# Optimization experiments

Measured on AMD Instinct MI355X. Metric: run time of the kernel, lower is better.

Reference implementation:

```python
import jax, jax.numpy as jnp
import numpy as np

FACTOR = 5

def setup_inputs() -> dict:
    key = jax.random.key(0)
    k1, k2, k3, k4 = jax.random.split(key, 4)
    B, L, E = 64, 4096, 64
    sample_k = min(FACTOR * int(np.ceil(np.log(L))), L)  # 45
    return {
        "queries": jax.random.normal(k1, (B, L, E), dtype=jnp.float32),
        "keys": jax.random.normal(k2, (B, L, E), dtype=jnp.float32),
        "values": jax.random.normal(k3, (B, L, E), dtype=jnp.float32),
        "index_sample": jax.random.randint(k4, (L, sample_k), 0, L, dtype=jnp.int32),
    }

def reference(queries, keys, values, index_sample):
    B, L_Q, D = queries.shape
    _, L_K, _ = keys.shape
    u = min(FACTOR * int(np.ceil(np.log(L_Q))), L_Q)  # n_top queries

    # --- _prob_QK: random K-sample gather + sparsity measure + topk ---
    # K_sample: (B, L_Q, sample_k, E) via gather (no dense K_expand materialized)
    K_sample = keys[:, index_sample, :]
    Q_K_sample = jnp.einsum('ble,blse->bls', queries, K_sample)
    M = Q_K_sample.max(-1) - Q_K_sample.sum(-1) / L_K  # (B, L_Q)
    _, M_top = jax.lax.top_k(M, u)  # (B, u) indices of top queries

    Q_reduce = jnp.take_along_axis(queries, M_top[:, :, None], axis=1)  # (B, u, E)
    scores_top = jnp.einsum('bue,bke->buk', Q_reduce, keys)  # (B, u, L_K)

    scale = 1.0 / np.sqrt(D)
    scores_top = scores_top * scale

    # --- _get_initial_context: mask_flag=True -> cumulative sum of V ---
    context = jnp.cumsum(values, axis=-2)  # (B, L_Q, D)

    # --- _update_context: softmax over full keys, scatter into context rows ---
    attn = jax.nn.softmax(scores_top, axis=-1)  # (B, u, L_K)
    upd = jnp.einsum('buk,bkd->bud', attn, values)  # (B, u, D)
    context = context.at[jnp.arange(B)[:, None], M_top, :].set(upd)
    return context
```

## Files before the change

### kernel.cpp

```cpp
#include <hip/hip_runtime.h>

#define Bv 64
#define Lv 4096
#define Dv 64
#define Uv 45
#define UP 48
#define NC 16
#define CKK 256
#define NSUB 64

#define OFF_M    0
#define SZ_M     (Bv*Lv)
#define OFF_QR   (OFF_M + SZ_M)
#define SZ_QR    (Bv*UP*Dv)
#define OFF_PMS  (OFF_QR + SZ_QR)
#define SZ_PMS   (Bv*NC*2*UP)
#define OFF_DEN  (OFF_PMS + SZ_PMS)
#define SZ_DEN   (Bv*2*UP)
#define OFF_PPV  (OFF_DEN + SZ_DEN)
#define SZ_PPV   (Bv*NC*UP*Dv)
#define OFF_CS   (OFF_PPV + SZ_PPV)
#define SZ_CS    (Bv*NSUB*Dv)
#define OFF_CO   (OFF_CS + SZ_CS)
#define SZ_CO    (Bv*NSUB*Dv)
#define OFF_TOP  (OFF_CO + SZ_CO)
#define SZ_TOP   (Bv*Uv)

__global__ __launch_bounds__(256) void k_M(const float* __restrict__ Q,
                                           const float* __restrict__ K,
                                           const int* __restrict__ idx,
                                           float* __restrict__ Mout) {
  __shared__ int sidx[16 * Uv];
  int i = blockIdx.x;
  int x = i & 7, j = i >> 3;
  int b = x + 8 * (j >> 8);
  int w = j & 255;
  int t = threadIdx.x;
  for (int p = t; p < 16 * Uv; p += 256) sidx[p] = idx[w * (16 * Uv) + p];
  int g = t >> 4, lane = t & 15;
  int l = w * 16 + g;
  float4 qv = *(const float4*)(Q + ((size_t)b * Lv + l) * Dv + lane * 4);
  const float* Kb = K + (size_t)b * Lv * Dv + lane * 4;
  __syncthreads();
  float mx = -3.0e38f, sm = 0.f;
#pragma unroll 5
  for (int s = 0; s < Uv; s++) {
    int ki = sidx[g * Uv + s];
    float4 kv = *(const float4*)(Kb + (size_t)ki * Dv);
    float d = qv.x * kv.x + qv.y * kv.y + qv.z * kv.z + qv.w * kv.w;
    d += __shfl_xor(d, 1);
    d += __shfl_xor(d, 2);
    d += __shfl_xor(d, 4);
    d += __shfl_xor(d, 8);
    mx = fmaxf(mx, d);
    sm += d;
  }
  if (lane == 0) Mout[(size_t)b * Lv + l] = mx - sm * (1.0f / (float)Lv);
}

__global__ __launch_bounds__(256) void k_topk(const float* __restrict__ M,
                                              int* __restrict__ Mtop) {
  __shared__ float sv[Lv];
  __shared__ float rmax[256];
  __shared__ int rind[256];
  int b = blockIdx.x;
  const float* Mb = M + (size_t)b * Lv;
  for (int i = threadIdx.x; i < Lv; i += 256) sv[i] = Mb[i];
  __syncthreads();
  for (int it = 0; it < Uv; it++) {
    float best = -3.0e38f; int bi = 1 << 30;
    for (int i = threadIdx.x; i < Lv; i += 256) {
      float v = sv[i];
      if (v > best) { best = v; bi = i; }
    }
    rmax[threadIdx.x] = best; rind[threadIdx.x] = bi;
    __syncthreads();
    for (int off = 128; off > 0; off >>= 1) {
      if (threadIdx.x < off) {
        float v2 = rmax[threadIdx.x + off]; int i2 = rind[threadIdx.x + off];
        if (v2 > rmax[threadIdx.x] ||
            (v2 == rmax[threadIdx.x] && i2 < rind[threadIdx.x])) {
          rmax[threadIdx.x] = v2; rind[threadIdx.x] = i2;
        }
      }
      __syncthreads();
    }
    if (threadIdx.x == 0) { Mtop[b * Uv + it] = rind[0]; sv[rind[0]] = -3.0e38f; }
    __syncthreads();
  }
}

__global__ __launch_bounds__(256) void k_qstage(const float* __restrict__ Q,
                                                const int* __restrict__ Mtop,
                                                float* __restrict__ Qr) {
  int b = blockIdx.x;
  for (int i = threadIdx.x; i < UP * Dv; i += 256) {
    int u = i >> 6, e = i & 63;
    float v = 0.f;
    if (u < Uv) {
      int row = Mtop[b * Uv + u];
      v = Q[((size_t)b * Lv + row) * Dv + e] * 0.125f;
    }
    Qr[((size_t)b * UP + u) * Dv + e] = v;
  }
}

#define STAGE_QST(QS, QR, b)                                        \
  for (int i_ = threadIdx.x; i_ < Dv * UP; i_ += blockDim.x) {      \
    int u_ = i_ >> 6, e_ = i_ & 63;                                 \
    QS[e_ * UP + u_] = QR[((size_t)(b) * UP + u_) * Dv + e_];       \
  }

#define SCORE_TILE(ACC, QS, KMAT, b_, c_, ug_, kg_)                                   \
  {                                                                                    \
    const float* Kb_ = (KMAT) + ((size_t)(b_) * Lv + (size_t)(c_) * CKK + (kg_)) * Dv; \
    for (int e = 0; e < Dv; e += 4) {                                                  \
      float qq[4][8];                                                                  \
      _Pragma("unroll")                                                                \
      for (int e2 = 0; e2 < 4; e2++) {                                                 \
        float4 qa = *(const float4*)&(QS)[(e + e2) * UP + (ug_) * 8];                  \
        float4 qb = *(const float4*)&(QS)[(e + e2) * UP + (ug_) * 8 + 4];              \
        qq[e2][0]=qa.x; qq[e2][1]=qa.y; qq[e2][2]=qa.z; qq[e2][3]=qa.w;                \
        qq[e2][4]=qb.x; qq[e2][5]=qb.y; qq[e2][6]=qb.z; qq[e2][7]=qb.w;                \
      }                                                                                \
      _Pragma("unroll")                                                                \
      for (int j = 0; j < 8; j++) {                                                    \
        float4 kv = *(const float4*)(Kb_ + (size_t)(32 * j) * Dv + e);                 \
        _Pragma("unroll")                                                              \
        for (int uu = 0; uu < 8; uu++)                                                 \
          ACC[uu][j] += qq[0][uu]*kv.x + qq[1][uu]*kv.y + qq[2][uu]*kv.z + qq[3][uu]*kv.w; \
      }                                                                                  \
    }                                                                                  \
  }

__global__ __launch_bounds__(192) void k_ms(const float* __restrict__ Kmat,
                                            const float* __restrict__ Qr,
                                            float* __restrict__ pms) {
  __shared__ float qsT[Dv * UP];
  int b = blockIdx.x >> 4, c = blockIdx.x & 15;
  STAGE_QST(qsT, Qr, b);
  __syncthreads();
  int t = threadIdx.x, ug = t >> 5, kg = t & 31;
  float acc[8][8];
#pragma unroll
  for (int uu = 0; uu < 8; uu++)
#pragma unroll
    for (int j = 0; j < 8; j++) acc[uu][j] = 0.f;
  SCORE_TILE(acc, qsT, Kmat, b, c, ug, kg);
#pragma unroll
  for (int uu = 0; uu < 8; uu++) {
    float m = acc[uu][0];
#pragma unroll
    for (int j = 1; j < 8; j++) m = fmaxf(m, acc[uu][j]);
#pragma unroll
    for (int off = 1; off < 32; off <<= 1) m = fmaxf(m, __shfl_xor(m, off));
    float s = 0.f;
#pragma unroll
    for (int j = 0; j < 8; j++) s += __expf(acc[uu][j] - m);
#pragma unroll
    for (int off = 1; off < 32; off <<= 1) s += __shfl_xor(s, off);
    if (kg == 0) {
      pms[(((size_t)b * NC + c) * 2 + 0) * UP + ug * 8 + uu] = m;
      pms[(((size_t)b * NC + c) * 2 + 1) * UP + ug * 8 + uu] = s;
    }
  }
}

__global__ __launch_bounds__(64) void k_den(const float* __restrict__ pms,
                                            float* __restrict__ den) {
  int b = blockIdx.x, u = threadIdx.x;
  if (u >= UP) return;
  float mx = -3.0e38f;
  for (int c = 0; c < NC; c++)
    mx = fmaxf(mx, pms[(((size_t)b * NC + c) * 2 + 0) * UP + u]);
  float d = 0.f;
  for (int c = 0; c < NC; c++)
    d += pms[(((size_t)b * NC + c) * 2 + 1) * UP + u] *
         __expf(pms[(((size_t)b * NC + c) * 2 + 0) * UP + u] - mx);
  den[(size_t)b * 2 * UP + u] = mx;
  den[(size_t)b * 2 * UP + UP + u] = 1.f / d;
}

__global__ __launch_bounds__(192) void k_pv(const float* __restrict__ Kmat,
                                            const float* __restrict__ V,
                                            const float* __restrict__ Qr,
                                            const float* __restrict__ den,
                                            float* __restrict__ ppv) {
  __shared__ float qsT[Dv * UP];
  __shared__ float wl[UP * CKK];
  int b = blockIdx.x >> 4, c = blockIdx.x & 15;
  STAGE_QST(qsT, Qr, b);
  __syncthreads();
  int t = threadIdx.x, ug = t >> 5, kg = t & 31;
  {
    float acc[8][8];
#pragma unroll
    for (int uu = 0; uu < 8; uu++)
#pragma unroll
      for (int j = 0; j < 8; j++) acc[uu][j] = 0.f;
    SCORE_TILE(acc, qsT, Kmat, b, c, ug, kg);
#pragma unroll
    for (int uu = 0; uu < 8; uu++) {
      float mx = den[(size_t)b * 2 * UP + ug * 8 + uu];
      float iv = den[(size_t)b * 2 * UP + UP + ug * 8 + uu];
#pragma unroll
      for (int j = 0; j < 8; j++)
        wl[(ug * 8 + uu) * CKK + kg + 32 * j] = __expf(acc[uu][j] - mx) * iv;
    }
  }
  __syncthreads();
  int w = t >> 6, lane = t & 63;
  float acc2[16];
#pragma unroll
  for (int uu = 0; uu < 16; uu++) acc2[uu] = 0.f;
  const float* Vb = V + ((size_t)b * Lv + (size_t)c * CKK) * Dv;
  for (int k4 = 0; k4 < CKK; k4 += 4) {
    float v0 = Vb[(size_t)(k4 + 0) * Dv + lane];
    float v1 = Vb[(size_t)(k4 + 1) * Dv + lane];
    float v2 = Vb[(size_t)(k4 + 2) * Dv + lane];
    float v3 = Vb[(size_t)(k4 + 3) * Dv + lane];
#pragma unroll
    for (int uu = 0; uu < 16; uu++) {
      float4 w4 = *(const float4*)&wl[(w * 16 + uu) * CKK + k4];
      acc2[uu] += w4.x * v0 + w4.y * v1 + w4.z * v2 + w4.w * v3;
    }
  }
#pragma unroll
  for (int uu = 0; uu < 16; uu++)
    ppv[(((size_t)b * NC + c) * UP + w * 16 + uu) * Dv + lane] = acc2[uu];
}

__global__ __launch_bounds__(256) void k_cs1(const float* __restrict__ V,
                                             float* __restrict__ cs) {
  int b = blockIdx.x >> 4, c4 = blockIdx.x & 15;
  int g = threadIdx.x >> 6, d = threadIdx.x & 63;
  int sub = c4 * 4 + g;
  const float* Vb = V + ((size_t)b * Lv + sub * 64) * Dv + d;
  float acc = 0.f;
  for (int r = 0; r < 64; r++) acc += Vb[(size_t)r * Dv];
  cs[((size_t)b * NSUB + sub) * Dv + d] = acc;
}

__global__ __launch_bounds__(64) void k_cs2(const float* __restrict__ cs,
                                            float* __restrict__ co) {
  int b = blockIdx.x, d = threadIdx.x;
  float run = 0.f;
  for (int s = 0; s < NSUB; s++) {
    co[((size_t)b * NSUB + s) * Dv + d] = run;
    run += cs[((size_t)b * NSUB + s) * Dv + d];
  }
}

__global__ __launch_bounds__(256) void k_cs3(const float* __restrict__ V,
                                             const float* __restrict__ co,
                                             float* __restrict__ out) {
  int b = blockIdx.x >> 4, c4 = blockIdx.x & 15;
  int g = threadIdx.x >> 6, d = threadIdx.x & 63;
  int sub = c4 * 4 + g;
  const float* Vb = V + ((size_t)b * Lv + sub * 64) * Dv + d;
  float* Ob = out + ((size_t)b * Lv + sub * 64) * Dv + d;
  float acc = co[((size_t)b * NSUB + sub) * Dv + d];
  for (int r = 0; r < 64; r++) {
    acc += Vb[(size_t)r * Dv];
    Ob[(size_t)r * Dv] = acc;
  }
}

__global__ __launch_bounds__(64) void k_upd(const float* __restrict__ ppv,
                                            const int* __restrict__ Mtop,
                                            float* __restrict__ out) {
  int b = blockIdx.x / Uv, u = blockIdx.x % Uv;
  int d = threadIdx.x;
  float s = 0.f;
  for (int c = 0; c < NC; c++)
    s += ppv[(((size_t)b * NC + c) * UP + u) * Dv + d];
  int row = Mtop[b * Uv + u];
  out[((size_t)b * Lv + row) * Dv + d] = s;
}

extern "C" void kernel_launch(void* const* d_in, const int* in_sizes, int n_in,
                              void* d_out, int out_size, void* d_ws, size_t ws_size,
                              hipStream_t stream) {
  (void)in_sizes; (void)n_in; (void)out_size; (void)ws_size;
  const float* Q = (const float*)d_in[0];
  const float* K = (const float*)d_in[1];
  const float* V = (const float*)d_in[2];
  const int* idx = (const int*)d_in[3];
  float* out = (float*)d_out;
  float* wsf = (float*)d_ws;
  float* M   = wsf + OFF_M;
  float* Qr  = wsf + OFF_QR;
  float* pms = wsf + OFF_PMS;
  float* den = wsf + OFF_DEN;
  float* ppv = wsf + OFF_PPV;
  float* cs  = wsf + OFF_CS;
  float* co  = wsf + OFF_CO;
  int* top   = (int*)(wsf + OFF_TOP);

  k_M<<<16384, 256, 0, stream>>>(Q, K, idx, M);
  k_topk<<<Bv, 256, 0, stream>>>(M, top);
  k_qstage<<<Bv, 256, 0, stream>>>(Q, top, Qr);
  k_ms<<<Bv * NC, 192, 0, stream>>>(K, Qr, pms);
  k_den<<<Bv, 64, 0, stream>>>(pms, den);
  k_pv<<<Bv * NC, 192, 0, stream>>>(K, V, Qr, den, ppv);
  k_cs1<<<1024, 256, 0, stream>>>(V, cs);
  k_cs2<<<Bv, 64, 0, stream>>>(cs, co);
  k_cs3<<<1024, 256, 0, stream>>>(V, co, out);
  k_upd<<<Bv * Uv, 64, 0, stream>>>(ppv, top, out);
}
```

Measured before the change: 630.3 us.

## Rewrite top-k with register/wave-shuffle reduction, fuse Q staging, drop cumsum pass

The top-k kernel now runs 1024 threads, keeps four M values per thread in registers, and reduces each iteration with wave shuffles plus a 16-entry cross-wave step, replacing the shared-memory tree reduction. It also gathers the selected query rows directly, removing the separate Q staging kernel. The sampled-score kernel now uses 8 lanes per query with two float4 loads each, which halves the block count and shortens the shuffle reduction. The middle cumsum kernel is removed, and each cs3 block recomputes its prefix offset by summing the earlier chunk sums, trading a little redundant reading for fewer launches.

Measured after the change: 596.3 us. 1.06x faster.

```diff
diff --git a/kernel.cpp b/kernel.cpp
--- a/kernel.cpp
+++ b/kernel.cpp
@@ -21,84 +21,98 @@
 #define SZ_PPV   (Bv*NC*UP*Dv)
 #define OFF_CS   (OFF_PPV + SZ_PPV)
 #define SZ_CS    (Bv*NSUB*Dv)
-#define OFF_CO   (OFF_CS + SZ_CS)
-#define SZ_CO    (Bv*NSUB*Dv)
-#define OFF_TOP  (OFF_CO + SZ_CO)
+#define OFF_TOP  (OFF_CS + SZ_CS)
 #define SZ_TOP   (Bv*Uv)
 
 __global__ __launch_bounds__(256) void k_M(const float* __restrict__ Q,
                                            const float* __restrict__ K,
                                            const int* __restrict__ idx,
                                            float* __restrict__ Mout) {
-  __shared__ int sidx[16 * Uv];
+  __shared__ int sidx[32 * Uv];
   int i = blockIdx.x;
   int x = i & 7, j = i >> 3;
-  int b = x + 8 * (j >> 8);
-  int w = j & 255;
+  int b = x + 8 * (j >> 7);
+  int w = j & 127;
   int t = threadIdx.x;
-  for (int p = t; p < 16 * Uv; p += 256) sidx[p] = idx[w * (16 * Uv) + p];
-  int g = t >> 4, lane = t & 15;
-  int l = w * 16 + g;
-  float4 qv = *(const float4*)(Q + ((size_t)b * Lv + l) * Dv + lane * 4);
-  const float* Kb = K + (size_t)b * Lv * Dv + lane * 4;
+  for (int p = t; p < 32 * Uv; p += 256) sidx[p] = idx[(w * 32) * Uv + p];
+  int g = t >> 3, lane = t & 7;
+  int l = w * 32 + g;
+  const float4* qr = (const float4*)(Q + ((size_t)b * Lv + l) * Dv + lane * 8);
+  float4 q0 = qr[0], q1 = qr[1];
+  const char* Kb = (const char*)(K + (size_t)b * Lv * Dv) + lane * 32;
   __syncthreads();
   float mx = -3.0e38f, sm = 0.f;
-#pragma unroll 5
+#pragma unroll 3
   for (int s = 0; s < Uv; s++) {
     int ki = sidx[g * Uv + s];
-    float4 kv = *(const float4*)(Kb + (size_t)ki * Dv);
-    float d = qv.x * kv.x + qv.y * kv.y + qv.z * kv.z + qv.w * kv.w;
+    const float4* kr = (const float4*)(Kb + (size_t)ki * 256);
+    float4 k0 = kr[0], k1 = kr[1];
+    float d = q0.x * k0.x + q0.y * k0.y + q0.z * k0.z + q0.w * k0.w
+            + q1.x * k1.x + q1.y * k1.y + q1.z * k1.z + q1.w * k1.w;
     d += __shfl_xor(d, 1);
     d += __shfl_xor(d, 2);
     d += __shfl_xor(d, 4);
-    d += __shfl_xor(d, 8);
     mx = fmaxf(mx, d);
     sm += d;
   }
   if (lane == 0) Mout[(size_t)b * Lv + l] = mx - sm * (1.0f / (float)Lv);
 }
 
-__global__ __launch_bounds__(256) void k_topk(const float* __restrict__ M,
-                                              int* __restrict__ Mtop) {
-  __shared__ float sv[Lv];
-  __shared__ float rmax[256];
-  __shared__ int rind[256];
+__global__ __launch_bounds__(1024) void k_topk(const float* __restrict__ M,
+                                               const float* __restrict__ Q,
+                                               int* __restrict__ Mtop,
+                                               float* __restrict__ Qr) {
+  __shared__ float wv[16];
+  __shared__ int wi[16];
+  __shared__ float win_v;
+  __shared__ int win_i;
+  __shared__ int list[Uv];
   int b = blockIdx.x;
+  int t = threadIdx.x;
   const float* Mb = M + (size_t)b * Lv;
-  for (int i = threadIdx.x; i < Lv; i += 256) sv[i] = Mb[i];
-  __syncthreads();
+  float r0 = Mb[t], r1 = Mb[t + 1024], r2 = Mb[t + 2048], r3 = Mb[t + 3072];
+  int wave = t >> 6, lane = t & 63;
   for (int it = 0; it < Uv; it++) {
-    float best = -3.0e38f; int bi = 1 << 30;
-    for (int i = threadIdx.x; i < Lv; i += 256) {
-      float v = sv[i];
-      if (v > best) { best = v; bi = i; }
-    }
-    rmax[threadIdx.x] = best; rind[threadIdx.x] = bi;
+    float bv = r0; int bi = t;
+    if (r1 > bv) { bv = r1; bi = t + 1024; }
+    if (r2 > bv) { bv = r2; bi = t + 2048; }
+    if (r3 > bv) { bv = r3; bi = t + 3072; }
+#pragma unroll
+    for (int off = 1; off < 64; off <<= 1) {
+      float v2 = __shfl_xor(bv, off);
+      int i2 = __shfl_xor(bi, off);
+      if (v2 > bv || (v2 == bv && i2 < bi)) { bv = v2; bi = i2; }
+    }
+    if (lane == 0) { wv[wave] = bv; wi[wave] = bi; }
     __syncthreads();
-    for (int off = 128; off > 0; off >>= 1) {
-      if (threadIdx.x < off) {
-        float v2 = rmax[threadIdx.x + off]; int i2 = rind[threadIdx.x + off];
-        if (v2 > rmax[threadIdx.x] ||
-            (v2 == rmax[threadIdx.x] && i2 < rind[threadIdx.x])) {
-          rmax[threadIdx.x] = v2; rind[threadIdx.x] = i2;
-        }
+    if (t < 64) {
+      float cv = (lane < 16) ? wv[lane] : -3.0e38f;
+      int ci = (lane < 16) ? wi[lane] : (1 << 30);
+#pragma unroll
+      for (int off = 1; off < 16; off <<= 1) {
+        float v2 = __shfl_xor(cv, off);
+        int i2 = __shfl_xor(ci, off);
+        if (v2 > cv || (v2 == cv && i2 < ci)) { cv = v2; ci = i2; }
       }
-      __syncthreads();
-    }
-    if (threadIdx.x == 0) { Mtop[b * Uv + it] = rind[0]; sv[rind[0]] = -3.0e38f; }
+      if (lane == 0) { win_v = cv; win_i = ci; list[it] = ci; }
+    }
     __syncthreads();
-  }
-}
-
-__global__ __launch_bounds__(256) void k_qstage(const float* __restrict__ Q,
-                                                const int* __restrict__ Mtop,
-                                                float* __restrict__ Qr) {
-  int b = blockIdx.x;
-  for (int i = threadIdx.x; i < UP * Dv; i += 256) {
-    int u = i >> 6, e = i & 63;
+    int wn = win_i;
+    if ((wn & 1023) == t) {
+      int c = wn >> 10;
+      if (c == 0) r0 = -3.0e38f;
+      else if (c == 1) r1 = -3.0e38f;
+      else if (c == 2) r2 = -3.0e38f;
+      else r3 = -3.0e38f;
+    }
+    __syncthreads();
+  }
+  if (t < Uv) Mtop[b * Uv + t] = list[t];
+  for (int p = t; p < UP * Dv; p += 1024) {
+    int u = p >> 6, e = p & 63;
     float v = 0.f;
     if (u < Uv) {
-      int row = Mtop[b * Uv + u];
+      int row = list[u];
       v = Q[((size_t)b * Lv + row) * Dv + e] * 0.125f;
     }
     Qr[((size_t)b * UP + u) * Dv + e] = v;
@@ -241,25 +255,16 @@
   cs[((size_t)b * NSUB + sub) * Dv + d] = acc;
 }
 
-__global__ __launch_bounds__(64) void k_cs2(const float* __restrict__ cs,
-                                            float* __restrict__ co) {
-  int b = blockIdx.x, d = threadIdx.x;
-  float run = 0.f;
-  for (int s = 0; s < NSUB; s++) {
-    co[((size_t)b * NSUB + s) * Dv + d] = run;
-    run += cs[((size_t)b * NSUB + s) * Dv + d];
-  }
-}
-
 __global__ __launch_bounds__(256) void k_cs3(const float* __restrict__ V,
-                                             const float* __restrict__ co,
+                                             const float* __restrict__ cs,
                                              float* __restrict__ out) {
   int b = blockIdx.x >> 4, c4 = blockIdx.x & 15;
   int g = threadIdx.x >> 6, d = threadIdx.x & 63;
   int sub = c4 * 4 + g;
+  float acc = 0.f;
+  for (int s = 0; s < sub; s++) acc += cs[((size_t)b * NSUB + s) * Dv + d];
   const float* Vb = V + ((size_t)b * Lv + sub * 64) * Dv + d;
   float* Ob = out + ((size_t)b * Lv + sub * 64) * Dv + d;
-  float acc = co[((size_t)b * NSUB + sub) * Dv + d];
   for (int r = 0; r < 64; r++) {
     acc += Vb[(size_t)r * Dv];
     Ob[(size_t)r * Dv] = acc;
@@ -294,17 +299,14 @@
   float* den = wsf + OFF_DEN;
   float* ppv = wsf + OFF_PPV;
   float* cs  = wsf + OFF_CS;
-  float* co  = wsf + OFF_CO;
   int* top   = (int*)(wsf + OFF_TOP);
 
-  k_M<<<16384, 256, 0, stream>>>(Q, K, idx, M);
-  k_topk<<<Bv, 256, 0, stream>>>(M, top);
-  k_qstage<<<Bv, 256, 0, stream>>>(Q, top, Qr);
+  k_M<<<8192, 256, 0, stream>>>(Q, K, idx, M);
+  k_topk<<<Bv, 1024, 0, stream>>>(M, Q, top, Qr);
   k_ms<<<Bv * NC, 192, 0, stream>>>(K, Qr, pms);
   k_den<<<Bv, 64, 0, stream>>>(pms, den);
   k_pv<<<Bv * NC, 192, 0, stream>>>(K, V, Qr, den, ppv);
   k_cs1<<<1024, 256, 0, stream>>>(V, cs);
-  k_cs2<<<Bv, 64, 0, stream>>>(cs, co);
-  k_cs3<<<1024, 256, 0, stream>>>(V, co, out);
+  k_cs3<<<1024, 256, 0, stream>>>(V, cs, out);
   k_upd<<<Bv * Uv, 64, 0, stream>>>(ppv, top, out);
 }
```
